# Kernel tuning notes

Hardware: AMD Instinct MI355X
Metric: run time of the kernel (lower is better)

## Reference

```python
import jax, jax.numpy as jnp
import numpy as np

GELU_C = 0.7978845608028654  # sqrt(2/pi)

def new_gelu(x):
    return 0.5 * x * (1.0 + jnp.tanh(GELU_C * (x + 0.044715 * x ** 3)))

def signed_quant(x, num_non_signbits, max_value):
    n = 2 ** num_non_signbits
    return jnp.sign(x) * jnp.minimum(jnp.round(jnp.abs(x) / max_value * n) + 1.0, float(n - 1))

def reverse_signed_quant(q, num_non_signbits, max_value):
    n = 2 ** num_non_signbits
    return jnp.sign(q) * (jnp.abs(q) - 1.0) / n * max_value

def setup_inputs() -> dict:
    key = jax.random.key(0)
    k1, k2, k3 = jax.random.split(key, 3)
    B, S, NX, NF = 4, 2048, 1024, 4096
    inp = jax.random.normal(k1, (B, S, NX), dtype=jnp.float32)
    weight = jax.random.normal(k2, (NX, NF), dtype=jnp.float32) * 0.02
    bias = jnp.zeros((NF,), dtype=jnp.float32)
    return {"input": inp, "weight": weight, "bias": bias}

def reference(input, weight, bias):
    # idx = 0 -> threshold=0.0, num_bits_to_calculate=3, weight bits=3
    threshold = 0.0
    num_bits = 3
    w_bits = 3
    max_input_value = 8.0
    nx = weight.shape[0]
    # per-input-row power-of-two weight scale: [nx, 1]
    max_weight_value = 2.0 ** jnp.round(jnp.log2(jnp.max(jnp.abs(weight), axis=-1, keepdims=True)))
    in_q = signed_quant(input, num_bits, max_input_value)
    w_q = signed_quant(weight, w_bits, max_weight_value)
    b_q = signed_quant(bias, num_bits, max_input_value)
    # low-precision prediction scores
    out_sign = (in_q @ w_q) / nx / (2.0 ** ((num_bits + w_bits) / 2))
    # dequantized approximate output + GELU
    out_rev = (reverse_signed_quant(in_q, num_bits, max_input_value)
               @ reverse_signed_quant(w_q, w_bits, max_weight_value)
               + reverse_signed_quant(b_q, num_bits, max_input_value))
    gelu_rev = new_gelu(out_rev)
    # full-precision path
    full = new_gelu(input @ weight + bias)
    return jnp.where(out_sign < threshold, gelu_rev, full)
```

## Files before the change

### kernel.cpp

```cpp
#include <hip/hip_runtime.h>
#include <hip/hip_bf16.h>

#define M_DIM 8192
#define K_DIM 1024
#define N_DIM 4096
#define BUF_BYTES 49152

typedef __attribute__((ext_vector_type(8))) short bf16x8;
typedef __attribute__((ext_vector_type(4))) int i32x4;
typedef __attribute__((ext_vector_type(16))) int i32x16;
typedef __attribute__((ext_vector_type(16))) float f32x16;

__device__ __forceinline__ short f2bf(float f) {
  unsigned u = __builtin_bit_cast(unsigned, f);
  u = (u + 0x7fffu + ((u >> 16) & 1u)) >> 16;
  return (short)u;
}

__device__ __forceinline__ unsigned f2fp8(float v) {
  unsigned b = __builtin_bit_cast(unsigned, v);
  unsigned sg = (b >> 24) & 0x80u;
  unsigned ab = b & 0x7fffffffu;
  if (ab == 0) return sg;
  int e = (int)(ab >> 23) - 127;
  unsigned m3 = (ab >> 20) & 7u;
  if (e >= -6) return sg | (unsigned)((e + 7) << 3) | m3;
  return sg | ((8u + m3) >> (-6 - e));
}

__device__ __forceinline__ float gelu_f(float x) {
  float u = 0.7978845608028654f * (x + 0.044715f * x * x * x);
  float e = __expf(2.0f * u);
  float t = 1.0f - 2.0f / (e + 1.0f);
  return 0.5f * x * (1.0f + t);
}

__device__ __forceinline__ void gload16(const void* g, void* l) {
  __builtin_amdgcn_global_load_lds((const __attribute__((address_space(1))) void*)g,
                                   (__attribute__((address_space(3))) void*)l, 16, 0, 0);
}

__global__ void rowmax_kernel(const float* __restrict__ w, float* __restrict__ mw) {
  int row = blockIdx.x * 4 + (threadIdx.x >> 6);
  int lane = threadIdx.x & 63;
  const float4* rp = (const float4*)(w + (size_t)row * N_DIM);
  float m = 0.0f;
#pragma unroll
  for (int it = 0; it < 16; ++it) {
    float4 v = rp[it * 64 + lane];
    m = fmaxf(m, fmaxf(fmaxf(fabsf(v.x), fabsf(v.y)), fmaxf(fabsf(v.z), fabsf(v.w))));
  }
#pragma unroll
  for (int off = 32; off > 0; off >>= 1) m = fmaxf(m, __shfl_xor(m, off, 64));
  if (lane == 0) mw[row] = exp2f(rintf(log2f(m)));
}

__global__ void prep_a_kernel(const float* __restrict__ inp, signed char* __restrict__ aqi,
                              unsigned char* __restrict__ adf, short* __restrict__ af) {
  int c = blockIdx.x * 256 + threadIdx.x;
  int kg = c >> 13, m = c & 8191;
  const float4* src = (const float4*)(inp + (size_t)m * K_DIM + kg * 16);
  float xs[16];
#pragma unroll
  for (int v = 0; v < 4; ++v) {
    float4 t = src[v];
    xs[v * 4 + 0] = t.x; xs[v * 4 + 1] = t.y; xs[v * 4 + 2] = t.z; xs[v * 4 + 3] = t.w;
  }
  int qi[4] = {0, 0, 0, 0};
  unsigned long long f8lo = 0ull, f8hi = 0ull;
  bf16x8 b0, b1;
#pragma unroll
  for (int j = 0; j < 16; ++j) {
    float x = xs[j];
    float s = (x > 0.f) ? 1.f : ((x < 0.f) ? -1.f : 0.f);
    float r = rintf(fabsf(x));
    int iq = (int)(s * fminf(r + 1.f, 7.f));
    qi[j >> 2] |= (iq & 255) << ((j & 3) * 8);
    unsigned f8 = f2fp8(s * fminf(r, 6.f));
    if (j < 8) f8lo |= (unsigned long long)f8 << (j * 8);
    else       f8hi |= (unsigned long long)f8 << ((j - 8) * 8);
    short bb = f2bf(x);
    if (j < 8) b0[j] = bb; else b1[j - 8] = bb;
  }
  *(i32x4*)(aqi + ((size_t)kg * M_DIM + m) * 16) = (i32x4){qi[0], qi[1], qi[2], qi[3]};
  *(unsigned long long*)(adf + ((size_t)(2 * kg) * M_DIM + m) * 8) = f8lo;
  *(unsigned long long*)(adf + ((size_t)(2 * kg + 1) * M_DIM + m) * 8) = f8hi;
  *(bf16x8*)(af + ((size_t)(2 * kg) * M_DIM + m) * 8) = b0;
  *(bf16x8*)(af + ((size_t)(2 * kg + 1) * M_DIM + m) * 8) = b1;
}

__global__ void prep_w_kernel(const float* __restrict__ w, const float* __restrict__ mw,
                              signed char* __restrict__ wqi, unsigned char* __restrict__ wdf,
                              short* __restrict__ wf) {
  int c = blockIdx.x * 256 + threadIdx.x;
  int kg = c >> 12, n = c & 4095;
  int qi[4] = {0, 0, 0, 0};
  unsigned long long f8lo = 0ull, f8hi = 0ull;
  bf16x8 b0, b1;
#pragma unroll
  for (int j = 0; j < 16; ++j) {
    float wv = w[(size_t)(kg * 16 + j) * N_DIM + n];
    float sc = mw[kg * 16 + j];
    float s = (wv > 0.f) ? 1.f : ((wv < 0.f) ? -1.f : 0.f);
    float r = rintf(fabsf(wv) * (8.0f / sc));
    int iq = (int)(s * fminf(r + 1.f, 7.f));
    qi[j >> 2] |= (iq & 255) << ((j & 3) * 8);
    unsigned f8 = f2fp8(s * fminf(r, 6.f) * 0.125f * sc);
    if (j < 8) f8lo |= (unsigned long long)f8 << (j * 8);
    else       f8hi |= (unsigned long long)f8 << ((j - 8) * 8);
    short bb = f2bf(wv);
    if (j < 8) b0[j] = bb; else b1[j - 8] = bb;
  }
  *(i32x4*)(wqi + ((size_t)kg * N_DIM + n) * 16) = (i32x4){qi[0], qi[1], qi[2], qi[3]};
  *(unsigned long long*)(wdf + ((size_t)(2 * kg) * N_DIM + n) * 8) = f8lo;
  *(unsigned long long*)(wdf + ((size_t)(2 * kg + 1) * N_DIM + n) * 8) = f8hi;
  *(bf16x8*)(wf + ((size_t)(2 * kg) * N_DIM + n) * 8) = b0;
  *(bf16x8*)(wf + ((size_t)(2 * kg + 1) * N_DIM + n) * 8) = b1;
}

__global__ __launch_bounds__(512, 2) void fused_gemm_kernel(
    const signed char* __restrict__ aqi, const unsigned char* __restrict__ adf,
    const short* __restrict__ af, const signed char* __restrict__ wqi,
    const unsigned char* __restrict__ wdf, const short* __restrict__ wf,
    const float* __restrict__ bias, float* __restrict__ out) {
  extern __shared__ char lds[];

  const int tid = threadIdx.x;
  const int wid = tid >> 6;
  const int lane = tid & 63;

  int bid = blockIdx.x;
  bid = (bid & 7) * 128 + (bid >> 3);
  const int bm0 = (bid >> 4) * 128;
  const int bn0 = (bid & 15) * 256;

  const int wr = wid >> 2;
  const int wc = wid & 3;

  const char* gb[6]; int gs[6]; int lo[6];
#pragma unroll
  for (int i = 0; i < 6; ++i) {
    int u = wid * 6 + i;
    lo[i] = u * 1024 + lane * 16;
    if (u < 4) {
      int o = u * 64 + lane; int kg = o >> 7, row = o & 127;
      gb[i] = (const char*)aqi + (size_t)(kg * M_DIM + bm0 + row) * 16;
      gs[i] = 32 * M_DIM;
    } else if (u < 8) {
      int kg = u - 4;
      gb[i] = (const char*)adf + (size_t)(kg * M_DIM + bm0) * 8 + lane * 16;
      gs[i] = 32 * M_DIM;
    } else if (u < 16) {
      int o = (u - 8) * 64 + lane; int kg = o >> 7, row = o & 127;
      gb[i] = (const char*)af + (size_t)(kg * M_DIM + bm0 + row) * 16;
      gs[i] = 64 * M_DIM;
    } else if (u < 24) {
      int o = (u - 16) * 64 + lane; int kg = o >> 8, col = o & 255;
      gb[i] = (const char*)wqi + (size_t)(kg * N_DIM + bn0 + col) * 16;
      gs[i] = 32 * N_DIM;
    } else if (u < 32) {
      int uu = u - 24; int kg = uu >> 1; int col = (uu & 1) * 128 + lane * 2;
      gb[i] = (const char*)wdf + (size_t)(kg * N_DIM + bn0 + col) * 8;
      gs[i] = 32 * N_DIM;
    } else {
      int o = (u - 32) * 64 + lane; int kg = o >> 8, col = o & 255;
      gb[i] = (const char*)wf + (size_t)(kg * N_DIM + bn0 + col) * 16;
      gs[i] = 64 * N_DIM;
    }
  }

  const int h = lane >> 5;
  const int l31 = lane & 31;
  const int ra = wr * 64 + l31;
  const int rb = wc * 64 + l31;

  i32x16 acc0[2][2];
  f32x16 acc1[2][2], acc2[2][2];
  const i32x16 zi = {0, 0, 0, 0, 0, 0, 0, 0, 0, 0, 0, 0, 0, 0, 0, 0};
  const f32x16 zf = {0, 0, 0, 0, 0, 0, 0, 0, 0, 0, 0, 0, 0, 0, 0, 0};
#pragma unroll
  for (int mf = 0; mf < 2; ++mf)
#pragma unroll
    for (int nf = 0; nf < 2; ++nf) { acc0[mf][nf] = zi; acc1[mf][nf] = zf; acc2[mf][nf] = zf; }

#pragma unroll
  for (int i = 0; i < 6; ++i) gload16(gb[i], lds + lo[i]);

  for (int t = 0; t < 32; ++t) {
    const int cb = (t & 1) * BUF_BYTES;
    if (t < 31) {
      const int nb = ((t + 1) & 1) * BUF_BYTES;
#pragma unroll
      for (int i = 0; i < 6; ++i)
        gload16(gb[i] + (size_t)(t + 1) * gs[i], lds + nb + lo[i]);
      asm volatile("s_waitcnt vmcnt(6)" ::: "memory");
    } else {
      asm volatile("s_waitcnt vmcnt(0)" ::: "memory");
    }
    __builtin_amdgcn_s_barrier();
    __builtin_amdgcn_sched_barrier(0);

    const char* B = lds + cb;
    {
      i32x4 a0[2], b0[2];
#pragma unroll
      for (int mf = 0; mf < 2; ++mf)
        a0[mf] = *(const i32x4*)(B + (h * 128 + ra + mf * 32) * 16);
#pragma unroll
      for (int nf = 0; nf < 2; ++nf)
        b0[nf] = *(const i32x4*)(B + 16384 + (h * 256 + rb + nf * 32) * 16);
#pragma unroll
      for (int mf = 0; mf < 2; ++mf)
#pragma unroll
        for (int nf = 0; nf < 2; ++nf)
          acc0[mf][nf] =
              __builtin_amdgcn_mfma_i32_32x32x32_i8(a0[mf], b0[nf], acc0[mf][nf], 0, 0, 0);
    }
#pragma unroll
    for (int kg = 0; kg < 2; ++kg) {
      long a1[2], b1[2];
#pragma unroll
      for (int mf = 0; mf < 2; ++mf)
        a1[mf] = *(const long*)(B + 4096 + ((kg * 2 + h) * 128 + ra + mf * 32) * 8);
#pragma unroll
      for (int nf = 0; nf < 2; ++nf)
        b1[nf] = *(const long*)(B + 24576 + ((kg * 2 + h) * 256 + rb + nf * 32) * 8);
#pragma unroll
      for (int mf = 0; mf < 2; ++mf)
#pragma unroll
        for (int nf = 0; nf < 2; ++nf)
          acc1[mf][nf] = __builtin_amdgcn_mfma_f32_32x32x16_fp8_fp8(a1[mf], b1[nf],
                                                                    acc1[mf][nf], 0, 0, 0);
    }
#pragma unroll
    for (int kg = 0; kg < 2; ++kg) {
      bf16x8 a2[2], b2[2];
#pragma unroll
      for (int mf = 0; mf < 2; ++mf)
        a2[mf] = *(const bf16x8*)(B + 8192 + ((kg * 2 + h) * 128 + ra + mf * 32) * 16);
#pragma unroll
      for (int nf = 0; nf < 2; ++nf)
        b2[nf] = *(const bf16x8*)(B + 32768 + ((kg * 2 + h) * 256 + rb + nf * 32) * 16);
#pragma unroll
      for (int mf = 0; mf < 2; ++mf)
#pragma unroll
        for (int nf = 0; nf < 2; ++nf)
          acc2[mf][nf] = __builtin_amdgcn_mfma_f32_32x32x16_bf16(a2[mf], b2[nf],
                                                                 acc2[mf][nf], 0, 0, 0);
    }
    asm volatile("s_waitcnt lgkmcnt(0)" ::: "memory");
    __builtin_amdgcn_sched_barrier(0);
    __builtin_amdgcn_s_barrier();
  }

#pragma unroll
  for (int nf = 0; nf < 2; ++nf) {
    const int col = bn0 + rb + nf * 32;
    const float bv = bias[col];
    const float sb = (bv > 0.f) ? 1.f : ((bv < 0.f) ? -1.f : 0.f);
    const float db = sb * fminf(rintf(fabsf(bv)), 6.f);
#pragma unroll
    for (int mf = 0; mf < 2; ++mf) {
#pragma unroll
      for (int r = 0; r < 16; ++r) {
        const int row = bm0 + wr * 64 + mf * 32 + (r & 3) + 8 * (r >> 2) + 4 * h;
        float x = (acc0[mf][nf][r] < 0) ? (acc1[mf][nf][r] + db) : (acc2[mf][nf][r] + bv);
        out[(size_t)row * N_DIM + col] = gelu_f(x);
      }
    }
  }
}

extern "C" void kernel_launch(void* const* d_in, const int* in_sizes, int n_in,
                              void* d_out, int out_size, void* d_ws, size_t ws_size,
                              hipStream_t stream) {
  const float* inp = (const float*)d_in[0];
  const float* w = (const float*)d_in[1];
  const float* bias = (const float*)d_in[2];
  float* out = (float*)d_out;

  char* p = (char*)d_ws;
  short* af = (short*)p;             p += (size_t)M_DIM * K_DIM * 2;
  short* wf = (short*)p;             p += (size_t)K_DIM * N_DIM * 2;
  signed char* aqi = (signed char*)p; p += (size_t)M_DIM * K_DIM;
  unsigned char* adf = (unsigned char*)p; p += (size_t)M_DIM * K_DIM;
  signed char* wqi = (signed char*)p; p += (size_t)K_DIM * N_DIM;
  unsigned char* wdf = (unsigned char*)p; p += (size_t)K_DIM * N_DIM;
  float* mw = (float*)p;

  const int lds_bytes = 2 * BUF_BYTES;
  hipFuncSetAttribute((const void*)fused_gemm_kernel,
                      hipFuncAttributeMaxDynamicSharedMemorySize, lds_bytes);

  rowmax_kernel<<<K_DIM / 4, 256, 0, stream>>>(w, mw);
  prep_a_kernel<<<(M_DIM * K_DIM / 16) / 256, 256, 0, stream>>>(inp, aqi, adf, af);
  prep_w_kernel<<<(K_DIM * N_DIM / 16) / 256, 256, 0, stream>>>(w, mw, wqi, wdf, wf);
  fused_gemm_kernel<<<(M_DIM / 128) * (N_DIM / 256), 512, lds_bytes, stream>>>(
      aqi, adf, af, wqi, wdf, wf, bias, out);
}
```

Measured before the change: 203.4 us.

## Shrink GEMM block tile to 128x128 with 4 waves and raise MFMA priority

Changes the fused triple-GEMM block tile from 128x256 with 8 waves to 128x128 with 4 waves. This halves the per-stage LDS buffer, doubles the grid, and remaps the global-to-LDS load assignment with eight loads per thread. The intent is more resident blocks per CU and better latency hiding. It also wraps the MFMA section in s_setprio to favour the compute waves. The cost is less reuse of the A operand per block, so A traffic from global memory/L2 doubles.

```diff
diff --git a/kernel.cpp b/kernel.cpp
--- a/kernel.cpp
+++ b/kernel.cpp
@@ -4,7 +4,7 @@
 #define M_DIM 8192
 #define K_DIM 1024
 #define N_DIM 4096
-#define BUF_BYTES 49152
+#define BUF_BYTES 32768
 
 typedef __attribute__((ext_vector_type(8))) short bf16x8;
 typedef __attribute__((ext_vector_type(4))) int i32x4;
@@ -118,7 +118,7 @@
   *(bf16x8*)(wf + ((size_t)(2 * kg + 1) * N_DIM + n) * 8) = b1;
 }
 
-__global__ __launch_bounds__(512, 2) void fused_gemm_kernel(
+__global__ __launch_bounds__(256, 2) void fused_gemm_kernel(
     const signed char* __restrict__ aqi, const unsigned char* __restrict__ adf,
     const short* __restrict__ af, const signed char* __restrict__ wqi,
     const unsigned char* __restrict__ wdf, const short* __restrict__ wf,
@@ -130,41 +130,41 @@
   const int lane = tid & 63;
 
   int bid = blockIdx.x;
-  bid = (bid & 7) * 128 + (bid >> 3);
-  const int bm0 = (bid >> 4) * 128;
-  const int bn0 = (bid & 15) * 256;
-
-  const int wr = wid >> 2;
-  const int wc = wid & 3;
-
-  const char* gb[6]; int gs[6]; int lo[6];
-#pragma unroll
-  for (int i = 0; i < 6; ++i) {
-    int u = wid * 6 + i;
+  bid = (bid & 7) * 256 + (bid >> 3);
+  const int bm0 = (bid >> 5) * 128;
+  const int bn0 = (bid & 31) * 128;
+
+  const int wr = wid >> 1;
+  const int wc = wid & 1;
+
+  const char* gb[8]; int gs[8]; int lo[8];
+#pragma unroll
+  for (int i = 0; i < 8; ++i) {
+    int u = wid * 8 + i;
     lo[i] = u * 1024 + lane * 16;
     if (u < 4) {
-      int o = u * 64 + lane; int kg = o >> 7, row = o & 127;
-      gb[i] = (const char*)aqi + (size_t)(kg * M_DIM + bm0 + row) * 16;
+      int o = u * 64 + lane; int h2 = o >> 7, row = o & 127;
+      gb[i] = (const char*)aqi + ((size_t)h2 * M_DIM + bm0 + row) * 16;
       gs[i] = 32 * M_DIM;
     } else if (u < 8) {
       int kg = u - 4;
-      gb[i] = (const char*)adf + (size_t)(kg * M_DIM + bm0) * 8 + lane * 16;
+      gb[i] = (const char*)adf + ((size_t)kg * M_DIM + bm0) * 8 + lane * 16;
       gs[i] = 32 * M_DIM;
     } else if (u < 16) {
       int o = (u - 8) * 64 + lane; int kg = o >> 7, row = o & 127;
-      gb[i] = (const char*)af + (size_t)(kg * M_DIM + bm0 + row) * 16;
+      gb[i] = (const char*)af + ((size_t)kg * M_DIM + bm0 + row) * 16;
       gs[i] = 64 * M_DIM;
+    } else if (u < 20) {
+      int o = (u - 16) * 64 + lane; int h2 = o >> 7, col = o & 127;
+      gb[i] = (const char*)wqi + ((size_t)h2 * N_DIM + bn0 + col) * 16;
+      gs[i] = 32 * N_DIM;
     } else if (u < 24) {
-      int o = (u - 16) * 64 + lane; int kg = o >> 8, col = o & 255;
-      gb[i] = (const char*)wqi + (size_t)(kg * N_DIM + bn0 + col) * 16;
-      gs[i] = 32 * N_DIM;
-    } else if (u < 32) {
-      int uu = u - 24; int kg = uu >> 1; int col = (uu & 1) * 128 + lane * 2;
-      gb[i] = (const char*)wdf + (size_t)(kg * N_DIM + bn0 + col) * 8;
+      int kg = u - 20;
+      gb[i] = (const char*)wdf + ((size_t)kg * N_DIM + bn0) * 8 + lane * 16;
       gs[i] = 32 * N_DIM;
     } else {
-      int o = (u - 32) * 64 + lane; int kg = o >> 8, col = o & 255;
-      gb[i] = (const char*)wf + (size_t)(kg * N_DIM + bn0 + col) * 16;
+      int o = (u - 24) * 64 + lane; int kg = o >> 7, col = o & 127;
+      gb[i] = (const char*)wf + ((size_t)kg * N_DIM + bn0 + col) * 16;
       gs[i] = 64 * N_DIM;
     }
   }
@@ -184,16 +184,16 @@
     for (int nf = 0; nf < 2; ++nf) { acc0[mf][nf] = zi; acc1[mf][nf] = zf; acc2[mf][nf] = zf; }
 
 #pragma unroll
-  for (int i = 0; i < 6; ++i) gload16(gb[i], lds + lo[i]);
+  for (int i = 0; i < 8; ++i) gload16(gb[i], lds + lo[i]);
 
   for (int t = 0; t < 32; ++t) {
     const int cb = (t & 1) * BUF_BYTES;
     if (t < 31) {
       const int nb = ((t + 1) & 1) * BUF_BYTES;
 #pragma unroll
-      for (int i = 0; i < 6; ++i)
+      for (int i = 0; i < 8; ++i)
         gload16(gb[i] + (size_t)(t + 1) * gs[i], lds + nb + lo[i]);
-      asm volatile("s_waitcnt vmcnt(6)" ::: "memory");
+      asm volatile("s_waitcnt vmcnt(8)" ::: "memory");
     } else {
       asm volatile("s_waitcnt vmcnt(0)" ::: "memory");
     }
@@ -201,6 +201,7 @@
     __builtin_amdgcn_sched_barrier(0);
 
     const char* B = lds + cb;
+    __builtin_amdgcn_s_setprio(1);
     {
       i32x4 a0[2], b0[2];
 #pragma unroll
@@ -208,7 +209,7 @@
         a0[mf] = *(const i32x4*)(B + (h * 128 + ra + mf * 32) * 16);
 #pragma unroll
       for (int nf = 0; nf < 2; ++nf)
-        b0[nf] = *(const i32x4*)(B + 16384 + (h * 256 + rb + nf * 32) * 16);
+        b0[nf] = *(const i32x4*)(B + 16384 + (h * 128 + rb + nf * 32) * 16);
 #pragma unroll
       for (int mf = 0; mf < 2; ++mf)
 #pragma unroll
@@ -217,14 +218,14 @@
               __builtin_amdgcn_mfma_i32_32x32x32_i8(a0[mf], b0[nf], acc0[mf][nf], 0, 0, 0);
     }
 #pragma unroll
-    for (int kg = 0; kg < 2; ++kg) {
+    for (int kk = 0; kk < 2; ++kk) {
       long a1[2], b1[2];
 #pragma unroll
       for (int mf = 0; mf < 2; ++mf)
-        a1[mf] = *(const long*)(B + 4096 + ((kg * 2 + h) * 128 + ra + mf * 32) * 8);
+        a1[mf] = *(const long*)(B + 4096 + ((kk * 2 + h) * 128 + ra + mf * 32) * 8);
 #pragma unroll
       for (int nf = 0; nf < 2; ++nf)
-        b1[nf] = *(const long*)(B + 24576 + ((kg * 2 + h) * 256 + rb + nf * 32) * 8);
+        b1[nf] = *(const long*)(B + 20480 + ((kk * 2 + h) * 128 + rb + nf * 32) * 8);
 #pragma unroll
       for (int mf = 0; mf < 2; ++mf)
 #pragma unroll
@@ -233,14 +234,14 @@
                                                                     acc1[mf][nf], 0, 0, 0);
     }
 #pragma unroll
-    for (int kg = 0; kg < 2; ++kg) {
+    for (int kk = 0; kk < 2; ++kk) {
       bf16x8 a2[2], b2[2];
 #pragma unroll
       for (int mf = 0; mf < 2; ++mf)
-        a2[mf] = *(const bf16x8*)(B + 8192 + ((kg * 2 + h) * 128 + ra + mf * 32) * 16);
+        a2[mf] = *(const bf16x8*)(B + 8192 + ((kk * 2 + h) * 128 + ra + mf * 32) * 16);
 #pragma unroll
       for (int nf = 0; nf < 2; ++nf)
-        b2[nf] = *(const bf16x8*)(B + 32768 + ((kg * 2 + h) * 256 + rb + nf * 32) * 16);
+        b2[nf] = *(const bf16x8*)(B + 24576 + ((kk * 2 + h) * 128 + rb + nf * 32) * 16);
 #pragma unroll
       for (int mf = 0; mf < 2; ++mf)
 #pragma unroll
@@ -248,6 +249,7 @@
           acc2[mf][nf] = __builtin_amdgcn_mfma_f32_32x32x16_bf16(a2[mf], b2[nf],
                                                                  acc2[mf][nf], 0, 0, 0);
     }
+    __builtin_amdgcn_s_setprio(0);
     asm volatile("s_waitcnt lgkmcnt(0)" ::: "memory");
     __builtin_amdgcn_sched_barrier(0);
     __builtin_amdgcn_s_barrier();
@@ -295,6 +297,6 @@
   rowmax_kernel<<<K_DIM / 4, 256, 0, stream>>>(w, mw);
   prep_a_kernel<<<(M_DIM * K_DIM / 16) / 256, 256, 0, stream>>>(inp, aqi, adf, af);
   prep_w_kernel<<<(K_DIM * N_DIM / 16) / 256, 256, 0, stream>>>(w, mw, wqi, wdf, wf);
-  fused_gemm_kernel<<<(M_DIM / 128) * (N_DIM / 256), 512, lds_bytes, stream>>>(
+  fused_gemm_kernel<<<(M_DIM / 128) * (N_DIM / 128), 256, lds_bytes, stream>>>(
       aqi, adf, af, wqi, wdf, wf, bias, out);
 }
```

Measured after the change: 213.0 us, median of 4. +4.7%, slower.
